# Optimization experiments

Measured on AMD Instinct MI355X. Metric: run time of the kernel, lower is better.

Reference implementation:

```python
import jax, jax.numpy as jnp
import numpy as np

N_NODES = 50000
N_EDGES = 600000
NUM_RELS = 5
IN_CH = 768
HID = 128
OUT_CH = 128
REL_DIM = 200


def _segment_softmax(scores, seg, n):
    # numerically stable softmax over variable-size segments (destination nodes)
    m = jax.ops.segment_max(scores, seg, num_segments=n)
    e = jnp.exp(scores - m[seg])
    s = jax.ops.segment_sum(e, seg, num_segments=n)
    return e / s[seg]


def _hgn_conv(x, edge_index, edge_type, W, Wr, a, Wres, rel_tab, final):
    # x: [N, h_in]; W: [h, h_in]; Wr: [h, rel_dim]; a: [3h]; rel_tab: [R, rel_dim]
    src = edge_index[0]
    dst = edge_index[1]
    n = x.shape[0]
    h = W.shape[0]
    Wx = x @ W.T                      # [N, h] (shared by x_i, x_j, messages)
    rel = rel_tab[edge_type] @ Wr.T   # [E, h]
    aA, aB, aC = a[:h], a[h:2 * h], a[2 * h:]
    # a([Wx_i | Wx_j | Wr rel]) decomposed to avoid materializing the concat
    score = Wx[dst] @ aA + Wx[src] @ aB + rel @ aC   # [E]
    alpha = jax.nn.leaky_relu(score, 0.2)
    alpha = _segment_softmax(alpha, dst, n)
    agg = jax.ops.segment_sum(Wx[src] * alpha[:, None], dst, num_segments=n)
    out = jax.nn.elu(agg + x @ Wres.T)
    if final:
        out = out / jnp.maximum(jnp.linalg.norm(out, axis=1, keepdims=True), 1e-12)
    return out, alpha


def setup_inputs() -> dict:
    key = jax.random.key(0)
    ks = jax.random.split(key, 20)
    s = 0.02
    return {
        "x": jax.random.normal(ks[0], (N_NODES, IN_CH), jnp.float32),
        "edge_index": jax.random.randint(ks[1], (2, N_EDGES), 0, N_NODES, jnp.int64 if jax.config.jax_enable_x64 else jnp.int32),
        "edge_type": jax.random.randint(ks[2], (N_EDGES,), 0, NUM_RELS, jnp.int64 if jax.config.jax_enable_x64 else jnp.int32),
        "l1_W": jax.random.normal(ks[3], (HID, IN_CH), jnp.float32) * s,
        "l1_b": jnp.zeros((HID,), jnp.float32),
        "l2_W": jax.random.normal(ks[4], (OUT_CH, HID), jnp.float32) * s,
        "l2_b": jnp.zeros((OUT_CH,), jnp.float32),
        "W1": jax.random.normal(ks[5], (HID, HID), jnp.float32) * s,
        "Wr1": jax.random.normal(ks[6], (HID, REL_DIM), jnp.float32) * s,
        "a1": jax.random.normal(ks[7], (3 * HID,), jnp.float32) * s,
        "Wres1": jax.random.normal(ks[8], (HID, HID), jnp.float32) * s,
        "rel1": jax.random.normal(ks[9], (NUM_RELS, REL_DIM), jnp.float32),
        "W2": jax.random.normal(ks[10], (HID, HID), jnp.float32) * s,
        "Wr2": jax.random.normal(ks[11], (HID, REL_DIM), jnp.float32) * s,
        "a2": jax.random.normal(ks[12], (3 * HID,), jnp.float32) * s,
        "Wres2": jax.random.normal(ks[13], (HID, HID), jnp.float32) * s,
        "rel2": jax.random.normal(ks[14], (NUM_RELS, REL_DIM), jnp.float32),
    }


def reference(x, edge_index, edge_type, l1_W, l1_b, l2_W, l2_b,
              W1, Wr1, a1, Wres1, rel1, W2, Wr2, a2, Wres2, rel2):
    out = jax.nn.leaky_relu(x @ l1_W.T + l1_b, 0.01)
    # layer 1 (dropout is identity in eval mode)
    out, alpha = _hgn_conv(out, edge_index, edge_type, W1, Wr1, a1, Wres1, rel1, final=False)
    # layer 2: original code blends alpha into self.alpha but weights messages
    # with its own (unblended) softmax alpha, so pre_alpha does not affect output
    out, _ = _hgn_conv(out, edge_index, edge_type, W2, Wr2, a2, Wres2, rel2, final=True)
    out = jax.nn.leaky_relu(out @ l2_W.T + l2_b, 0.01)
    return out
```

## Files before the change

### kernel.cpp

```cpp
#include <hip/hip_runtime.h>

namespace {

typedef unsigned short ushort_t;
typedef unsigned int uint_t;
typedef __attribute__((ext_vector_type(8))) short bf16x8;
typedef __attribute__((ext_vector_type(4))) float f32x4;

constexpr int N   = 50000;
constexpr int E   = 600000;
constexpr int NR  = 5;
constexpr int KIN = 768;
constexpr int H   = 128;
constexpr int RD  = 200;

__device__ inline ushort_t f2b(float f){
  uint_t u = __builtin_bit_cast(uint_t, f);
  uint_t r = (u + 0x7FFFu + ((u >> 16) & 1u)) >> 16;
  return (ushort_t)r;
}
__device__ inline float b2f_lo(uint_t u){ return __builtin_bit_cast(float, u << 16); }
__device__ inline float b2f_hi(uint_t u){ return __builtin_bit_cast(float, u & 0xFFFF0000u); }
__device__ inline float b2f_us(ushort_t h){ return __builtin_bit_cast(float, ((uint_t)h) << 16); }
__device__ inline uint_t cvtpk(float lo, float hi){
  uint_t r;
  asm("v_cvt_pk_bf16_f32 %0, %1, %2" : "=v"(r) : "v"(lo), "v"(hi));
  return r;
}

__global__ void prep_k(const float* __restrict__ l1W, const float* __restrict__ W1,
                       const float* __restrict__ R1, const float* __restrict__ W2,
                       const float* __restrict__ R2, const float* __restrict__ l2W,
                       ushort_t* __restrict__ wts, int* __restrict__ deg,
                       const float* __restrict__ rel1, const float* __restrict__ Wr1,
                       const float* __restrict__ a1, float* __restrict__ sC1,
                       const float* __restrict__ rel2, const float* __restrict__ Wr2,
                       const float* __restrict__ a2, float* __restrict__ sC2){
  constexpr int S0 = H * KIN;
  constexpr int S1 = H * H;
  int b = blockIdx.x, tid = threadIdx.x;
  if (b < 704){
    int i = b * 256 + tid;
    float v;
    if (i < S0) v = l1W[i];
    else {
      int j = i - S0, seg = j >> 14, off = j & (S1 - 1);
      const float* srcs[5] = {W1, R1, W2, R2, l2W};
      v = srcs[seg][off];
    }
    wts[i] = f2b(v);
  } else if (b < 900){
    int i = (b - 704) * 256 + tid;
    if (i < N) deg[i] = 0;
  } else {
    int L = b - 900;
    const float* rel = L ? rel2 : rel1;
    const float* Wr  = L ? Wr2  : Wr1;
    const float* a   = L ? a2   : a1;
    float*       sC  = L ? sC2  : sC1;
    __shared__ float red[256];
    int n = tid >> 1, half = tid & 1;
    float aC = a[256 + n];
    for (int r = 0; r < NR; ++r){
      float p = 0.f;
      for (int k = half * 100; k < half * 100 + 100; ++k)
        p += rel[r * RD + k] * Wr[n * RD + k];
      red[tid] = p * aC;
      __syncthreads();
      for (int s = 128; s > 0; s >>= 1){
        if (tid < s) red[tid] += red[tid + s];
        __syncthreads();
      }
      if (tid == 0) sC[r] = red[0];
      __syncthreads();
    }
  }
}

__global__ void degcount_k(const int* __restrict__ dst, int* __restrict__ deg){
  int e = blockIdx.x * 256 + threadIdx.x;
  if (e < E) atomicAdd(&deg[dst[e]], 1);
}

__global__ void scan1_k(const int* __restrict__ deg, int* __restrict__ chunk,
                        int* __restrict__ bsums, int n){
  __shared__ int s[256];
  int tid = threadIdx.x, i = blockIdx.x * 256 + tid;
  int v = (i < n) ? deg[i] : 0;
  s[tid] = v; __syncthreads();
  for (int off = 1; off < 256; off <<= 1){
    int t = (tid >= off) ? s[tid - off] : 0;
    __syncthreads();
    s[tid] += t;
    __syncthreads();
  }
  if (i < n) chunk[i] = s[tid] - v;
  if (tid == 255) bsums[blockIdx.x] = s[255];
}

__global__ void scan2_k(const int* __restrict__ bsums, int* __restrict__ boffs, int nb){
  __shared__ int s[256];
  int tid = threadIdx.x;
  int v = (tid < nb) ? bsums[tid] : 0;
  s[tid] = v; __syncthreads();
  for (int off = 1; off < 256; off <<= 1){
    int t = (tid >= off) ? s[tid - off] : 0;
    __syncthreads();
    s[tid] += t;
    __syncthreads();
  }
  if (tid < nb) boffs[tid] = s[tid] - v;
}

__global__ void scan3_k(int* __restrict__ rowptr, const int* __restrict__ boffs,
                        int* __restrict__ cursor, int n, int total){
  int i = blockIdx.x * 256 + threadIdx.x;
  if (i < n){
    int v = rowptr[i] + boffs[blockIdx.x];
    rowptr[i] = v; cursor[i] = v;
  }
  if (i == 0) rowptr[n] = total;
}

__global__ void fill_k(const int* __restrict__ src, const int* __restrict__ dst,
                       const int* __restrict__ et, int* __restrict__ cursor,
                       int* __restrict__ cpk){
  int e = blockIdx.x * 256 + threadIdx.x;
  if (e < E){
    int d = dst[e];
    int p = atomicAdd(&cursor[d], 1);
    cpk[p] = src[e] | (et[e] << 16);
  }
}

template<int K1, int M1, bool AFP32, bool NORM, bool STORE1, int M2>
__global__ __launch_bounds__(256) void gfused_k(
    const void* __restrict__ Ap, const ushort_t* __restrict__ Wb1,
    const float* __restrict__ bias1, const ushort_t* __restrict__ aggM,
    ushort_t* __restrict__ out1,
    const ushort_t* __restrict__ Wb2, const float* __restrict__ vec2,
    void* __restrict__ out2, float* __restrict__ sA, float* __restrict__ sB, int M)
{
  constexpr int AP = 40;
  constexpr int BP = 40;
  constexpr int CP = 136;
  __shared__ __align__(16) ushort_t U[128 * CP];
  __shared__ __align__(16) ushort_t Cs[64 * CP];
  ushort_t* const As  = U;
  ushort_t* const Bs  = U + 64 * AP;
  ushort_t* const B2s = U;
  const int tid  = threadIdx.x;
  const int wave = tid >> 6, lane = tid & 63;
  const int l15  = lane & 15, quad = lane >> 4;
  const int row0 = blockIdx.x * 64;

  if (M1 == 2){
    #pragma unroll
    for (int i = 0; i < 4; ++i){
      int idx = tid + 256 * i;
      int r = idx >> 4, c8 = idx & 15;
      int grow = row0 + r;
      uint4 v = make_uint4(0, 0, 0, 0);
      if (grow < M) v = *reinterpret_cast<const uint4*>(aggM + (size_t)grow * 128 + c8 * 8);
      *reinterpret_cast<uint4*>(&Cs[r * CP + c8 * 8]) = v;
    }
  }

  f32x4 acc[8];
  #pragma unroll
  for (int t = 0; t < 8; ++t) acc[t] = (f32x4){0.f, 0.f, 0.f, 0.f};

  const int ar = tid >> 2, aq = tid & 3;
  const int agrow = row0 + ar;
  const bool aok = agrow < M;
  const int bn = tid >> 1, bs16 = (tid & 1) * 16;

  float4 pf0 = make_float4(0.f, 0.f, 0.f, 0.f), pf1 = pf0;
  uint4  pu  = make_uint4(0, 0, 0, 0);
  uint4  pb0, pb1;

  if (AFP32){
    if (aok){
      const float* ap = (const float*)Ap + (size_t)agrow * K1 + aq * 8;
      pf0 = *reinterpret_cast<const float4*>(ap);
      pf1 = *reinterpret_cast<const float4*>(ap + 4);
    }
  } else if (aok){
    pu = *reinterpret_cast<const uint4*>((const ushort_t*)Ap + (size_t)agrow * K1 + aq * 8);
  }
  {
    const ushort_t* wp = Wb1 + (size_t)bn * K1 + bs16;
    pb0 = *reinterpret_cast<const uint4*>(wp);
    pb1 = *reinterpret_cast<const uint4*>(wp + 8);
  }

  for (int k0 = 0; k0 < K1; k0 += 32){
    uint4 av;
    if (AFP32){
      av.x = cvtpk(pf0.x, pf0.y); av.y = cvtpk(pf0.z, pf0.w);
      av.z = cvtpk(pf1.x, pf1.y); av.w = cvtpk(pf1.z, pf1.w);
    } else av = pu;
    *reinterpret_cast<uint4*>(&As[ar * AP + aq * 8]) = av;
    *reinterpret_cast<uint4*>(&Bs[bn * BP + bs16])     = pb0;
    *reinterpret_cast<uint4*>(&Bs[bn * BP + bs16 + 8]) = pb1;
    __syncthreads();
    if (k0 + 32 < K1){
      const int k1 = k0 + 32;
      if (AFP32){
        if (aok){
          const float* ap = (const float*)Ap + (size_t)agrow * K1 + k1 + aq * 8;
          pf0 = *reinterpret_cast<const float4*>(ap);
          pf1 = *reinterpret_cast<const float4*>(ap + 4);
        }
      } else if (aok){
        pu = *reinterpret_cast<const uint4*>((const ushort_t*)Ap + (size_t)agrow * K1 + k1 + aq * 8);
      }
      const ushort_t* wp = Wb1 + (size_t)bn * K1 + k1 + bs16;
      pb0 = *reinterpret_cast<const uint4*>(wp);
      pb1 = *reinterpret_cast<const uint4*>(wp + 8);
    }
    bf16x8 af = *reinterpret_cast<const bf16x8*>(&As[(wave * 16 + l15) * AP + quad * 8]);
    #pragma unroll
    for (int t = 0; t < 8; ++t){
      bf16x8 bfr = *reinterpret_cast<const bf16x8*>(&Bs[(t * 16 + l15) * BP + quad * 8]);
      acc[t] = __builtin_amdgcn_mfma_f32_16x16x32_bf16(af, bfr, acc[t], 0, 0, 0);
    }
    __syncthreads();
  }

  uint4 wreg[8];
  #pragma unroll
  for (int i = 0; i < 8; ++i){
    int idx = tid + 256 * i;
    int rr = idx >> 4, c8 = idx & 15;
    wreg[i] = *reinterpret_cast<const uint4*>(Wb2 + (size_t)rr * 128 + c8 * 8);
  }

  float vv[8][4];
  #pragma unroll
  for (int t = 0; t < 8; ++t){
    #pragma unroll
    for (int r = 0; r < 4; ++r){
      int lr  = wave * 16 + quad * 4 + r;
      int col = t * 16 + l15;
      float v = acc[t][r];
      if (M1 == 1){
        v += bias1[col];
        v = v > 0.f ? v : 0.01f * v;
      } else {
        v += b2f_us(Cs[lr * CP + col]);
        v = v > 0.f ? v : __expf(v) - 1.f;
      }
      vv[t][r] = v;
    }
  }
  #pragma unroll
  for (int i = 0; i < 8; ++i){
    int idx = tid + 256 * i;
    int rr = idx >> 4, c8 = idx & 15;
    *reinterpret_cast<uint4*>(&B2s[rr * CP + c8 * 8]) = wreg[i];
  }
  if (NORM){
    #pragma unroll
    for (int r = 0; r < 4; ++r){
      float ss = 0.f;
      #pragma unroll
      for (int t = 0; t < 8; ++t) ss += vv[t][r] * vv[t][r];
      #pragma unroll
      for (int off = 1; off < 16; off <<= 1) ss += __shfl_xor(ss, off, 64);
      float sc = 1.f / fmaxf(sqrtf(ss), 1e-12f);
      #pragma unroll
      for (int t = 0; t < 8; ++t) vv[t][r] *= sc;
    }
  }
  #pragma unroll
  for (int t = 0; t < 8; t += 2){
    #pragma unroll
    for (int r = 0; r < 4; ++r){
      int lr  = wave * 16 + quad * 4 + r;
      int c0  = t * 16 + l15, c1 = c0 + 16;
      uint_t pr = cvtpk(vv[t][r], vv[t + 1][r]);
      Cs[lr * CP + c0] = (ushort_t)pr;
      Cs[lr * CP + c1] = (ushort_t)(pr >> 16);
      if (STORE1){
        int grow = row0 + lr;
        if (grow < M){
          out1[(size_t)grow * 128 + c0] = (ushort_t)pr;
          out1[(size_t)grow * 128 + c1] = (ushort_t)(pr >> 16);
        }
      }
    }
  }
  __syncthreads();

  #pragma unroll
  for (int t = 0; t < 8; ++t) acc[t] = (f32x4){0.f, 0.f, 0.f, 0.f};
  #pragma unroll
  for (int kk = 0; kk < 4; ++kk){
    bf16x8 af2 = *reinterpret_cast<const bf16x8*>(&Cs[(wave * 16 + l15) * CP + kk * 32 + quad * 8]);
    #pragma unroll
    for (int t = 0; t < 8; ++t){
      bf16x8 bfr = *reinterpret_cast<const bf16x8*>(&B2s[(t * 16 + l15) * CP + kk * 32 + quad * 8]);
      acc[t] = __builtin_amdgcn_mfma_f32_16x16x32_bf16(af2, bfr, acc[t], 0, 0, 0);
    }
  }

  if (M2 == 1){
    #pragma unroll
    for (int t = 0; t < 8; ++t){
      #pragma unroll
      for (int r = 0; r < 4; ++r){
        int grow = row0 + wave * 16 + quad * 4 + r;
        if (grow >= M) continue;
        int col = t * 16 + l15;
        float v = acc[t][r] + vec2[col];
        v = v > 0.f ? v : 0.01f * v;
        ((float*)out2)[(size_t)grow * 128 + col] = v;
      }
    }
  } else {
    #pragma unroll
    for (int t = 0; t < 8; t += 2){
      #pragma unroll
      for (int r = 0; r < 4; ++r){
        int grow = row0 + wave * 16 + quad * 4 + r;
        if (grow >= M) continue;
        int c0 = t * 16 + l15;
        uint_t pr = cvtpk(acc[t][r], acc[t + 1][r]);
        ((ushort_t*)out2)[(size_t)grow * 128 + c0]      = (ushort_t)pr;
        ((ushort_t*)out2)[(size_t)grow * 128 + c0 + 16] = (ushort_t)(pr >> 16);
      }
    }
    #pragma unroll
    for (int r = 0; r < 4; ++r){
      float pa = 0.f, pb = 0.f;
      #pragma unroll
      for (int t = 0; t < 8; ++t){
        int col = t * 16 + l15;
        pa += acc[t][r] * vec2[col];
        pb += acc[t][r] * vec2[128 + col];
      }
      #pragma unroll
      for (int off = 1; off < 16; off <<= 1){
        pa += __shfl_xor(pa, off, 64);
        pb += __shfl_xor(pb, off, 64);
      }
      int grow = row0 + wave * 16 + quad * 4 + r;
      if (l15 == r && grow < M){ sA[grow] = pa; sB[grow] = pb; }
    }
  }
}

__global__ __launch_bounds__(256) void agg_k(
    const ushort_t* __restrict__ Wx, const float* __restrict__ sA,
    const float* __restrict__ sB, const float* __restrict__ sC,
    const int* __restrict__ rowptr, const int* __restrict__ cpk,
    uint_t* __restrict__ aggU, int n)
{
  const int node  = blockIdx.x * 16 + (threadIdx.x >> 4);
  const int l     = threadIdx.x & 15;
  const int gbase = threadIdx.x & 48;
  if (node >= n) return;
  int p0 = rowptr[node], p1 = rowptr[node + 1];
  int deg = p1 - p0;
  float sa = sA[node];
  float m = -1e30f, ssum = 0.f;
  float a[8];
  #pragma unroll
  for (int j = 0; j < 8; ++j) a[j] = 0.f;

  for (int c0 = 0; c0 < deg; c0 += 16){
    int cnt = deg - c0; if (cnt > 16) cnt = 16;
    bool ok = l < cnt;
    int pk = cpk[p0 + c0 + (ok ? l : 0)];
    float s = sa + sB[pk & 0xFFFF] + sC[pk >> 16];
    s = s > 0.f ? s : 0.2f * s;
    float sv = ok ? s : -1e30f;
    #pragma unroll
    for (int off = 8; off > 0; off >>= 1) sv = fmaxf(sv, __shfl_xor(sv, off, 16));
    float mn = fmaxf(m, sv);
    float corr = __expf(m - mn);
    ssum *= corr;
    #pragma unroll
    for (int j = 0; j < 8; ++j) a[j] *= corr;
    float ev = ok ? __expf(s - mn) : 0.f;
    float es = ev;
    #pragma unroll
    for (int off = 8; off > 0; off >>= 1) es += __shfl_xor(es, off, 16);
    ssum += es;
    m = mn;
    int png = ok ? pk : 0;

    for (int e = 0; e < cnt; e += 4){
      int b0l = gbase + e;
      int pe0 = __shfl(png, b0l,     64), pe1 = __shfl(png, b0l + 1, 64);
      int pe2 = __shfl(png, b0l + 2, 64), pe3 = __shfl(png, b0l + 3, 64);
      float e0 = __shfl(ev, b0l,     64), e1 = __shfl(ev, b0l + 1, 64);
      float e2 = __shfl(ev, b0l + 2, 64), e3 = __shfl(ev, b0l + 3, 64);
      uint4 u0 = *reinterpret_cast<const uint4*>(Wx + (size_t)(pe0 & 0xFFFF) * 128 + l * 8);
      uint4 u1 = *reinterpret_cast<const uint4*>(Wx + (size_t)(pe1 & 0xFFFF) * 128 + l * 8);
      uint4 u2 = *reinterpret_cast<const uint4*>(Wx + (size_t)(pe2 & 0xFFFF) * 128 + l * 8);
      uint4 u3 = *reinterpret_cast<const uint4*>(Wx + (size_t)(pe3 & 0xFFFF) * 128 + l * 8);
      a[0] += e0 * b2f_lo(u0.x); a[1] += e0 * b2f_hi(u0.x);
      a[2] += e0 * b2f_lo(u0.y); a[3] += e0 * b2f_hi(u0.y);
      a[4] += e0 * b2f_lo(u0.z); a[5] += e0 * b2f_hi(u0.z);
      a[6] += e0 * b2f_lo(u0.w); a[7] += e0 * b2f_hi(u0.w);
      a[0] += e1 * b2f_lo(u1.x); a[1] += e1 * b2f_hi(u1.x);
      a[2] += e1 * b2f_lo(u1.y); a[3] += e1 * b2f_hi(u1.y);
      a[4] += e1 * b2f_lo(u1.z); a[5] += e1 * b2f_hi(u1.z);
      a[6] += e1 * b2f_lo(u1.w); a[7] += e1 * b2f_hi(u1.w);
      a[0] += e2 * b2f_lo(u2.x); a[1] += e2 * b2f_hi(u2.x);
      a[2] += e2 * b2f_lo(u2.y); a[3] += e2 * b2f_hi(u2.y);
      a[4] += e2 * b2f_lo(u2.z); a[5] += e2 * b2f_hi(u2.z);
      a[6] += e2 * b2f_lo(u2.w); a[7] += e2 * b2f_hi(u2.w);
      a[0] += e3 * b2f_lo(u3.x); a[1] += e3 * b2f_hi(u3.x);
      a[2] += e3 * b2f_lo(u3.y); a[3] += e3 * b2f_hi(u3.y);
      a[4] += e3 * b2f_lo(u3.z); a[5] += e3 * b2f_hi(u3.z);
      a[6] += e3 * b2f_lo(u3.w); a[7] += e3 * b2f_hi(u3.w);
    }
  }
  float inv = (deg > 0) ? 1.f / ssum : 0.f;
  uint4 o;
  o.x = cvtpk(a[0] * inv, a[1] * inv);
  o.y = cvtpk(a[2] * inv, a[3] * inv);
  o.z = cvtpk(a[4] * inv, a[5] * inv);
  o.w = cvtpk(a[6] * inv, a[7] * inv);
  *reinterpret_cast<uint4*>(aggU + (size_t)node * 64 + l * 4) = o;
}

}

extern "C" void kernel_launch(void* const* d_in, const int* in_sizes, int n_in,
                              void* d_out, int out_size, void* d_ws, size_t ws_size,
                              hipStream_t stream)
{
  const float* x     = (const float*)d_in[0];
  const int*   eidx  = (const int*)d_in[1];
  const int*   et    = (const int*)d_in[2];
  const float* l1W   = (const float*)d_in[3];
  const float* l1b   = (const float*)d_in[4];
  const float* l2W   = (const float*)d_in[5];
  const float* l2b   = (const float*)d_in[6];
  const float* W1    = (const float*)d_in[7];
  const float* Wr1   = (const float*)d_in[8];
  const float* a1    = (const float*)d_in[9];
  const float* Wres1 = (const float*)d_in[10];
  const float* rel1  = (const float*)d_in[11];
  const float* W2    = (const float*)d_in[12];
  const float* Wr2   = (const float*)d_in[13];
  const float* a2    = (const float*)d_in[14];
  const float* Wres2 = (const float*)d_in[15];
  const float* rel2  = (const float*)d_in[16];
  float* outp = (float*)d_out;

  const int* esrc = eidx;
  const int* edst = eidx + E;

  float* f = (float*)d_ws;
  size_t o = 0;
  float* sA   = f + o; o += N;
  float* sB   = f + o; o += N;
  float* sC1  = f + o; o += 8;
  float* sC2  = f + o; o += 8;
  ushort_t* us = (ushort_t*)(f + o);
  size_t ou = 0;
  ushort_t* b0   = us + ou; ou += (size_t)N * H;
  ushort_t* b1   = us + ou; ou += (size_t)N * H;
  ushort_t* Wxb  = us + ou; ou += (size_t)N * H;
  ushort_t* aggB = us + ou; ou += (size_t)N * H;
  ushort_t* wtsb = us + ou; ou += (size_t)H * KIN + 5 * H * H;
  ushort_t* l1Wb = wtsb;
  ushort_t* W1b  = wtsb + H * KIN;
  ushort_t* R1b  = W1b + H * H;
  ushort_t* W2b  = R1b + H * H;
  ushort_t* R2b  = W2b + H * H;
  ushort_t* l2Wb = R2b + H * H;
  if (ou & 1) ou += 1;
  int* wi = (int*)(us + ou);
  size_t oi = 0;
  int* deg    = wi + oi; oi += N;
  int* rowptr = wi + oi; oi += N + 1;
  int* cursor = wi + oi; oi += N;
  int* bsums  = wi + oi; oi += 256;
  int* boffs  = wi + oi; oi += 256;
  int* cpk    = wi + oi; oi += E;

  const int EB    = (E + 255) / 256;
  const int NB256 = (N + 255) / 256;
  const int GB    = (N + 63) / 64;
  const int NB16  = (N + 15) / 16;

  prep_k<<<902, 256, 0, stream>>>(l1W, W1, Wres1, W2, Wres2, l2W, wtsb, deg,
                                  rel1, Wr1, a1, sC1, rel2, Wr2, a2, sC2);
  degcount_k<<<EB, 256, 0, stream>>>(edst, deg);
  scan1_k<<<NB256, 256, 0, stream>>>(deg, rowptr, bsums, N);
  scan2_k<<<1, 256, 0, stream>>>(bsums, boffs, NB256);
  scan3_k<<<NB256, 256, 0, stream>>>(rowptr, boffs, cursor, N, E);
  fill_k<<<EB, 256, 0, stream>>>(esrc, edst, et, cursor, cpk);

  gfused_k<KIN, 1, true, false, true, 3><<<GB, 256, 0, stream>>>(
      x, l1Wb, l1b, nullptr, b0, W1b, a1, Wxb, sA, sB, N);
  agg_k<<<NB16, 256, 0, stream>>>(Wxb, sA, sB, sC1, rowptr, cpk, (uint_t*)aggB, N);

  gfused_k<H, 2, false, false, true, 3><<<GB, 256, 0, stream>>>(
      b0, R1b, nullptr, aggB, b1, W2b, a2, Wxb, sA, sB, N);
  agg_k<<<NB16, 256, 0, stream>>>(Wxb, sA, sB, sC2, rowptr, cpk, (uint_t*)aggB, N);

  gfused_k<H, 2, false, true, false, 1><<<GB, 256, 0, stream>>>(
      b1, R2b, nullptr, aggB, nullptr, l2Wb, l2b, outp, nullptr, nullptr, N);
}
```

Before: 495.0 us.

## Load GEMM operands directly from global into MFMA registers, drop LDS staging

```diff
diff --git a/kernel.cpp b/kernel.cpp
--- a/kernel.cpp
+++ b/kernel.cpp
@@ -134,131 +134,74 @@
 }
 
 template<int K1, int M1, bool AFP32, bool NORM, bool STORE1, int M2>
-__global__ __launch_bounds__(256) void gfused_k(
+__global__ __launch_bounds__(256, 3) void gfused_k(
     const void* __restrict__ Ap, const ushort_t* __restrict__ Wb1,
     const float* __restrict__ bias1, const ushort_t* __restrict__ aggM,
     ushort_t* __restrict__ out1,
     const ushort_t* __restrict__ Wb2, const float* __restrict__ vec2,
     void* __restrict__ out2, float* __restrict__ sA, float* __restrict__ sB, int M)
 {
-  constexpr int AP = 40;
-  constexpr int BP = 40;
-  constexpr int CP = 136;
-  __shared__ __align__(16) ushort_t U[128 * CP];
-  __shared__ __align__(16) ushort_t Cs[64 * CP];
-  ushort_t* const As  = U;
-  ushort_t* const Bs  = U + 64 * AP;
-  ushort_t* const B2s = U;
+  __shared__ __align__(16) ushort_t Cs[64 * 128];
   const int tid  = threadIdx.x;
   const int wave = tid >> 6, lane = tid & 63;
   const int l15  = lane & 15, quad = lane >> 4;
   const int row0 = blockIdx.x * 64;
-
-  if (M1 == 2){
-    #pragma unroll
-    for (int i = 0; i < 4; ++i){
-      int idx = tid + 256 * i;
-      int r = idx >> 4, c8 = idx & 15;
-      int grow = row0 + r;
-      uint4 v = make_uint4(0, 0, 0, 0);
-      if (grow < M) v = *reinterpret_cast<const uint4*>(aggM + (size_t)grow * 128 + c8 * 8);
-      *reinterpret_cast<uint4*>(&Cs[r * CP + c8 * 8]) = v;
-    }
-  }
+  const int arow_l = wave * 16 + l15;
+  int ar = row0 + arow_l; if (ar >= M) ar = M - 1;
 
   f32x4 acc[8];
   #pragma unroll
   for (int t = 0; t < 8; ++t) acc[t] = (f32x4){0.f, 0.f, 0.f, 0.f};
 
-  const int ar = tid >> 2, aq = tid & 3;
-  const int agrow = row0 + ar;
-  const bool aok = agrow < M;
-  const int bn = tid >> 1, bs16 = (tid & 1) * 16;
-
-  float4 pf0 = make_float4(0.f, 0.f, 0.f, 0.f), pf1 = pf0;
-  uint4  pu  = make_uint4(0, 0, 0, 0);
-  uint4  pb0, pb1;
-
+  const ushort_t* wb = Wb1 + (size_t)l15 * K1 + quad * 8;
   if (AFP32){
-    if (aok){
-      const float* ap = (const float*)Ap + (size_t)agrow * K1 + aq * 8;
-      pf0 = *reinterpret_cast<const float4*>(ap);
-      pf1 = *reinterpret_cast<const float4*>(ap + 4);
-    }
-  } else if (aok){
-    pu = *reinterpret_cast<const uint4*>((const ushort_t*)Ap + (size_t)agrow * K1 + aq * 8);
-  }
-  {
-    const ushort_t* wp = Wb1 + (size_t)bn * K1 + bs16;
-    pb0 = *reinterpret_cast<const uint4*>(wp);
-    pb1 = *reinterpret_cast<const uint4*>(wp + 8);
-  }
-
-  for (int k0 = 0; k0 < K1; k0 += 32){
-    uint4 av;
-    if (AFP32){
-      av.x = cvtpk(pf0.x, pf0.y); av.y = cvtpk(pf0.z, pf0.w);
-      av.z = cvtpk(pf1.x, pf1.y); av.w = cvtpk(pf1.z, pf1.w);
-    } else av = pu;
-    *reinterpret_cast<uint4*>(&As[ar * AP + aq * 8]) = av;
-    *reinterpret_cast<uint4*>(&Bs[bn * BP + bs16])     = pb0;
-    *reinterpret_cast<uint4*>(&Bs[bn * BP + bs16 + 8]) = pb1;
-    __syncthreads();
-    if (k0 + 32 < K1){
-      const int k1 = k0 + 32;
-      if (AFP32){
-        if (aok){
-          const float* ap = (const float*)Ap + (size_t)agrow * K1 + k1 + aq * 8;
-          pf0 = *reinterpret_cast<const float4*>(ap);
-          pf1 = *reinterpret_cast<const float4*>(ap + 4);
-        }
-      } else if (aok){
-        pu = *reinterpret_cast<const uint4*>((const ushort_t*)Ap + (size_t)agrow * K1 + k1 + aq * 8);
-      }
-      const ushort_t* wp = Wb1 + (size_t)bn * K1 + k1 + bs16;
-      pb0 = *reinterpret_cast<const uint4*>(wp);
-      pb1 = *reinterpret_cast<const uint4*>(wp + 8);
-    }
-    bf16x8 af = *reinterpret_cast<const bf16x8*>(&As[(wave * 16 + l15) * AP + quad * 8]);
-    #pragma unroll
-    for (int t = 0; t < 8; ++t){
-      bf16x8 bfr = *reinterpret_cast<const bf16x8*>(&Bs[(t * 16 + l15) * BP + quad * 8]);
-      acc[t] = __builtin_amdgcn_mfma_f32_16x16x32_bf16(af, bfr, acc[t], 0, 0, 0);
-    }
-    __syncthreads();
-  }
-
-  uint4 wreg[8];
-  #pragma unroll
-  for (int i = 0; i < 8; ++i){
-    int idx = tid + 256 * i;
-    int rr = idx >> 4, c8 = idx & 15;
-    wreg[i] = *reinterpret_cast<const uint4*>(Wb2 + (size_t)rr * 128 + c8 * 8);
-  }
-
+    const float* ap = (const float*)Ap + (size_t)ar * K1 + quad * 8;
+    #pragma unroll 2
+    for (int k0 = 0; k0 < K1; k0 += 32){
+      float4 u0 = *reinterpret_cast<const float4*>(ap + k0);
+      float4 u1 = *reinterpret_cast<const float4*>(ap + k0 + 4);
+      uint4 av;
+      av.x = cvtpk(u0.x, u0.y); av.y = cvtpk(u0.z, u0.w);
+      av.z = cvtpk(u1.x, u1.y); av.w = cvtpk(u1.z, u1.w);
+      bf16x8 af = __builtin_bit_cast(bf16x8, av);
+      #pragma unroll
+      for (int t = 0; t < 8; ++t){
+        bf16x8 bfr = *reinterpret_cast<const bf16x8*>(wb + (size_t)t * 16 * K1 + k0);
+        acc[t] = __builtin_amdgcn_mfma_f32_16x16x32_bf16(af, bfr, acc[t], 0, 0, 0);
+      }
+    }
+  } else {
+    const ushort_t* apb = (const ushort_t*)Ap + (size_t)ar * K1 + quad * 8;
+    #pragma unroll 2
+    for (int k0 = 0; k0 < K1; k0 += 32){
+      bf16x8 af = *reinterpret_cast<const bf16x8*>(apb + k0);
+      #pragma unroll
+      for (int t = 0; t < 8; ++t){
+        bf16x8 bfr = *reinterpret_cast<const bf16x8*>(wb + (size_t)t * 16 * K1 + k0);
+        acc[t] = __builtin_amdgcn_mfma_f32_16x16x32_bf16(af, bfr, acc[t], 0, 0, 0);
+      }
+    }
+  }
+
+  const int lr0 = wave * 16 + quad * 4;
   float vv[8][4];
   #pragma unroll
   for (int t = 0; t < 8; ++t){
     #pragma unroll
     for (int r = 0; r < 4; ++r){
-      int lr  = wave * 16 + quad * 4 + r;
       int col = t * 16 + l15;
       float v = acc[t][r];
       if (M1 == 1){
         v += bias1[col];
         v = v > 0.f ? v : 0.01f * v;
       } else {
-        v += b2f_us(Cs[lr * CP + col]);
+        int g = row0 + lr0 + r;
+        float ag = (g < M) ? b2f_us(aggM[(size_t)g * 128 + col]) : 0.f;
+        v += ag;
         v = v > 0.f ? v : __expf(v) - 1.f;
       }
       vv[t][r] = v;
     }
-  }
-  #pragma unroll
-  for (int i = 0; i < 8; ++i){
-    int idx = tid + 256 * i;
-    int rr = idx >> 4, c8 = idx & 15;
-    *reinterpret_cast<uint4*>(&B2s[rr * CP + c8 * 8]) = wreg[i];
   }
   if (NORM){
     #pragma unroll
@@ -277,16 +220,18 @@
   for (int t = 0; t < 8; t += 2){
     #pragma unroll
     for (int r = 0; r < 4; ++r){
-      int lr  = wave * 16 + quad * 4 + r;
-      int c0  = t * 16 + l15, c1 = c0 + 16;
+      int row = lr0 + r;
+      int key = row & 7;
       uint_t pr = cvtpk(vv[t][r], vv[t + 1][r]);
-      Cs[lr * CP + c0] = (ushort_t)pr;
-      Cs[lr * CP + c1] = (ushort_t)(pr >> 16);
+      int c0 = t * 16 + l15, c1 = c0 + 16;
+      int p0 = ((c0 >> 3) ^ key) << 3, p1 = ((c1 >> 3) ^ key) << 3;
+      Cs[row * 128 + p0 + (l15 & 7)] = (ushort_t)pr;
+      Cs[row * 128 + p1 + (l15 & 7)] = (ushort_t)(pr >> 16);
       if (STORE1){
-        int grow = row0 + lr;
-        if (grow < M){
-          out1[(size_t)grow * 128 + c0] = (ushort_t)pr;
-          out1[(size_t)grow * 128 + c1] = (ushort_t)(pr >> 16);
+        int g = row0 + row;
+        if (g < M){
+          out1[(size_t)g * 128 + c0] = (ushort_t)pr;
+          out1[(size_t)g * 128 + c1] = (ushort_t)(pr >> 16);
         }
       }
     }
@@ -295,22 +240,28 @@
 
   #pragma unroll
   for (int t = 0; t < 8; ++t) acc[t] = (f32x4){0.f, 0.f, 0.f, 0.f};
-  #pragma unroll
-  for (int kk = 0; kk < 4; ++kk){
-    bf16x8 af2 = *reinterpret_cast<const bf16x8*>(&Cs[(wave * 16 + l15) * CP + kk * 32 + quad * 8]);
+  {
+    const int rr   = wave * 16 + l15;
+    const int rkey = l15 & 7;
+    const ushort_t* w2 = Wb2 + (size_t)l15 * 128 + quad * 8;
+    #pragma unroll 2
+    for (int kk = 0; kk < 4; ++kk){
+      int ph = (((kk * 4 + quad) ^ rkey) << 3);
+      bf16x8 af2 = *reinterpret_cast<const bf16x8*>(&Cs[rr * 128 + ph]);
+      #pragma unroll
+      for (int t = 0; t < 8; ++t){
+        bf16x8 bfr = *reinterpret_cast<const bf16x8*>(w2 + (size_t)t * 16 * 128 + kk * 32);
+        acc[t] = __builtin_amdgcn_mfma_f32_16x16x32_bf16(af2, bfr, acc[t], 0, 0, 0);
+      }
+    }
+  }
+
+  if (M2 == 1){
     #pragma unroll
     for (int t = 0; t < 8; ++t){
-      bf16x8 bfr = *reinterpret_cast<const bf16x8*>(&B2s[(t * 16 + l15) * CP + kk * 32 + quad * 8]);
-      acc[t] = __builtin_amdgcn_mfma_f32_16x16x32_bf16(af2, bfr, acc[t], 0, 0, 0);
-    }
-  }
-
-  if (M2 == 1){
-    #pragma unroll
-    for (int t = 0; t < 8; ++t){
       #pragma unroll
       for (int r = 0; r < 4; ++r){
-        int grow = row0 + wave * 16 + quad * 4 + r;
+        int grow = row0 + lr0 + r;
         if (grow >= M) continue;
         int col = t * 16 + l15;
         float v = acc[t][r] + vec2[col];
@@ -323,7 +274,7 @@
     for (int t = 0; t < 8; t += 2){
       #pragma unroll
       for (int r = 0; r < 4; ++r){
-        int grow = row0 + wave * 16 + quad * 4 + r;
+        int grow = row0 + lr0 + r;
         if (grow >= M) continue;
         int c0 = t * 16 + l15;
         uint_t pr = cvtpk(acc[t][r], acc[t + 1][r]);
@@ -345,7 +296,7 @@
         pa += __shfl_xor(pa, off, 64);
         pb += __shfl_xor(pb, off, 64);
       }
-      int grow = row0 + wave * 16 + quad * 4 + r;
+      int grow = row0 + lr0 + r;
       if (l15 == r && grow < M){ sA[grow] = pa; sB[grow] = pb; }
     }
   }
```

Measured after the change: 575.2 us. +16.2%, slower.

## Fuse edge softmax aggregation into the following GEMM kernel and merge degree count into prep

Applied to the files above, without the earlier changes.

```diff
diff --git a/kernel.cpp b/kernel.cpp
--- a/kernel.cpp
+++ b/kernel.cpp
@@ -32,6 +32,7 @@
                        const float* __restrict__ R1, const float* __restrict__ W2,
                        const float* __restrict__ R2, const float* __restrict__ l2W,
                        ushort_t* __restrict__ wts, int* __restrict__ deg,
+                       const int* __restrict__ edst,
                        const float* __restrict__ rel1, const float* __restrict__ Wr1,
                        const float* __restrict__ a1, float* __restrict__ sC1,
                        const float* __restrict__ rel2, const float* __restrict__ Wr2,
@@ -49,11 +50,8 @@
       v = srcs[seg][off];
     }
     wts[i] = f2b(v);
-  } else if (b < 900){
-    int i = (b - 704) * 256 + tid;
-    if (i < N) deg[i] = 0;
-  } else {
-    int L = b - 900;
+  } else if (b < 706){
+    int L = b - 704;
     const float* rel = L ? rel2 : rel1;
     const float* Wr  = L ? Wr2  : Wr1;
     const float* a   = L ? a2   : a1;
@@ -74,12 +72,10 @@
       if (tid == 0) sC[r] = red[0];
       __syncthreads();
     }
-  }
-}
-
-__global__ void degcount_k(const int* __restrict__ dst, int* __restrict__ deg){
-  int e = blockIdx.x * 256 + threadIdx.x;
-  if (e < E) atomicAdd(&deg[dst[e]], 1);
+  } else {
+    int e = (b - 706) * 256 + tid;
+    if (e < E) atomicAdd(&deg[edst[e]], 1);
+  }
 }
 
 __global__ void scan1_k(const int* __restrict__ deg, int* __restrict__ chunk,
@@ -136,10 +132,13 @@
 template<int K1, int M1, bool AFP32, bool NORM, bool STORE1, int M2>
 __global__ __launch_bounds__(256) void gfused_k(
     const void* __restrict__ Ap, const ushort_t* __restrict__ Wb1,
-    const float* __restrict__ bias1, const ushort_t* __restrict__ aggM,
+    const float* __restrict__ bias1,
+    const ushort_t* __restrict__ WxG, const int* __restrict__ rowptr,
+    const int* __restrict__ cpk, const float* __restrict__ sAi,
+    const float* __restrict__ sBi, const float* __restrict__ sCi,
     ushort_t* __restrict__ out1,
     const ushort_t* __restrict__ Wb2, const float* __restrict__ vec2,
-    void* __restrict__ out2, float* __restrict__ sA, float* __restrict__ sB, int M)
+    void* __restrict__ out2, float* __restrict__ sAo, float* __restrict__ sBo, int M)
 {
   constexpr int AP = 40;
   constexpr int BP = 40;
@@ -155,14 +154,78 @@
   const int row0 = blockIdx.x * 64;
 
   if (M1 == 2){
-    #pragma unroll
-    for (int i = 0; i < 4; ++i){
-      int idx = tid + 256 * i;
-      int r = idx >> 4, c8 = idx & 15;
-      int grow = row0 + r;
-      uint4 v = make_uint4(0, 0, 0, 0);
-      if (grow < M) v = *reinterpret_cast<const uint4*>(aggM + (size_t)grow * 128 + c8 * 8);
-      *reinterpret_cast<uint4*>(&Cs[r * CP + c8 * 8]) = v;
+    const int grp = tid >> 4;
+    const int l   = tid & 15;
+    const int gb  = tid & 48;
+    #pragma unroll 1
+    for (int nb = 0; nb < 4; ++nb){
+      int lrow = nb * 16 + grp;
+      int node = row0 + lrow;
+      uint4 o = make_uint4(0, 0, 0, 0);
+      if (node < M){
+        int p0 = rowptr[node], p1 = rowptr[node + 1];
+        int dg = p1 - p0;
+        float sa = sAi[node];
+        float m = -1e30f, ssum = 0.f;
+        float a[8];
+        #pragma unroll
+        for (int j = 0; j < 8; ++j) a[j] = 0.f;
+        for (int c0 = 0; c0 < dg; c0 += 16){
+          int cnt = dg - c0; if (cnt > 16) cnt = 16;
+          bool ok = l < cnt;
+          int pk = cpk[p0 + c0 + (ok ? l : 0)];
+          float s = sa + sBi[pk & 0xFFFF] + sCi[pk >> 16];
+          s = s > 0.f ? s : 0.2f * s;
+          float sv = ok ? s : -1e30f;
+          #pragma unroll
+          for (int off = 8; off > 0; off >>= 1) sv = fmaxf(sv, __shfl_xor(sv, off, 16));
+          float mn = fmaxf(m, sv);
+          float corr = __expf(m - mn);
+          ssum *= corr;
+          #pragma unroll
+          for (int j = 0; j < 8; ++j) a[j] *= corr;
+          float ev = ok ? __expf(s - mn) : 0.f;
+          float es = ev;
+          #pragma unroll
+          for (int off = 8; off > 0; off >>= 1) es += __shfl_xor(es, off, 16);
+          ssum += es;
+          m = mn;
+          int png = ok ? pk : 0;
+          for (int e = 0; e < cnt; e += 4){
+            int b0l = gb + e;
+            int pe0 = __shfl(png, b0l,     64), pe1 = __shfl(png, b0l + 1, 64);
+            int pe2 = __shfl(png, b0l + 2, 64), pe3 = __shfl(png, b0l + 3, 64);
+            float e0 = __shfl(ev, b0l,     64), e1 = __shfl(ev, b0l + 1, 64);
+            float e2 = __shfl(ev, b0l + 2, 64), e3 = __shfl(ev, b0l + 3, 64);
+            uint4 u0 = *reinterpret_cast<const uint4*>(WxG + (size_t)(pe0 & 0xFFFF) * 128 + l * 8);
+            uint4 u1 = *reinterpret_cast<const uint4*>(WxG + (size_t)(pe1 & 0xFFFF) * 128 + l * 8);
+            uint4 u2 = *reinterpret_cast<const uint4*>(WxG + (size_t)(pe2 & 0xFFFF) * 128 + l * 8);
+            uint4 u3 = *reinterpret_cast<const uint4*>(WxG + (size_t)(pe3 & 0xFFFF) * 128 + l * 8);
+            a[0] += e0 * b2f_lo(u0.x); a[1] += e0 * b2f_hi(u0.x);
+            a[2] += e0 * b2f_lo(u0.y); a[3] += e0 * b2f_hi(u0.y);
+            a[4] += e0 * b2f_lo(u0.z); a[5] += e0 * b2f_hi(u0.z);
+            a[6] += e0 * b2f_lo(u0.w); a[7] += e0 * b2f_hi(u0.w);
+            a[0] += e1 * b2f_lo(u1.x); a[1] += e1 * b2f_hi(u1.x);
+            a[2] += e1 * b2f_lo(u1.y); a[3] += e1 * b2f_hi(u1.y);
+            a[4] += e1 * b2f_lo(u1.z); a[5] += e1 * b2f_hi(u1.z);
+            a[6] += e1 * b2f_lo(u1.w); a[7] += e1 * b2f_hi(u1.w);
+            a[0] += e2 * b2f_lo(u2.x); a[1] += e2 * b2f_hi(u2.x);
+            a[2] += e2 * b2f_lo(u2.y); a[3] += e2 * b2f_hi(u2.y);
+            a[4] += e2 * b2f_lo(u2.z); a[5] += e2 * b2f_hi(u2.z);
+            a[6] += e2 * b2f_lo(u2.w); a[7] += e2 * b2f_hi(u2.w);
+            a[0] += e3 * b2f_lo(u3.x); a[1] += e3 * b2f_hi(u3.x);
+            a[2] += e3 * b2f_lo(u3.y); a[3] += e3 * b2f_hi(u3.y);
+            a[4] += e3 * b2f_lo(u3.z); a[5] += e3 * b2f_hi(u3.z);
+            a[6] += e3 * b2f_lo(u3.w); a[7] += e3 * b2f_hi(u3.w);
+          }
+        }
+        float inv = (dg > 0) ? 1.f / ssum : 0.f;
+        o.x = cvtpk(a[0] * inv, a[1] * inv);
+        o.y = cvtpk(a[2] * inv, a[3] * inv);
+        o.z = cvtpk(a[4] * inv, a[5] * inv);
+        o.w = cvtpk(a[6] * inv, a[7] * inv);
+      }
+      *reinterpret_cast<uint4*>(&Cs[lrow * CP + l * 8]) = o;
     }
   }
 
@@ -346,86 +409,9 @@
         pb += __shfl_xor(pb, off, 64);
       }
       int grow = row0 + wave * 16 + quad * 4 + r;
-      if (l15 == r && grow < M){ sA[grow] = pa; sB[grow] = pb; }
-    }
-  }
-}
-
-__global__ __launch_bounds__(256) void agg_k(
-    const ushort_t* __restrict__ Wx, const float* __restrict__ sA,
-    const float* __restrict__ sB, const float* __restrict__ sC,
-    const int* __restrict__ rowptr, const int* __restrict__ cpk,
-    uint_t* __restrict__ aggU, int n)
-{
-  const int node  = blockIdx.x * 16 + (threadIdx.x >> 4);
-  const int l     = threadIdx.x & 15;
-  const int gbase = threadIdx.x & 48;
-  if (node >= n) return;
-  int p0 = rowptr[node], p1 = rowptr[node + 1];
-  int deg = p1 - p0;
-  float sa = sA[node];
-  float m = -1e30f, ssum = 0.f;
-  float a[8];
-  #pragma unroll
-  for (int j = 0; j < 8; ++j) a[j] = 0.f;
-
-  for (int c0 = 0; c0 < deg; c0 += 16){
-    int cnt = deg - c0; if (cnt > 16) cnt = 16;
-    bool ok = l < cnt;
-    int pk = cpk[p0 + c0 + (ok ? l : 0)];
-    float s = sa + sB[pk & 0xFFFF] + sC[pk >> 16];
-    s = s > 0.f ? s : 0.2f * s;
-    float sv = ok ? s : -1e30f;
-    #pragma unroll
-    for (int off = 8; off > 0; off >>= 1) sv = fmaxf(sv, __shfl_xor(sv, off, 16));
-    float mn = fmaxf(m, sv);
-    float corr = __expf(m - mn);
-    ssum *= corr;
-    #pragma unroll
-    for (int j = 0; j < 8; ++j) a[j] *= corr;
-    float ev = ok ? __expf(s - mn) : 0.f;
-    float es = ev;
-    #pragma unroll
-    for (int off = 8; off > 0; off >>= 1) es += __shfl_xor(es, off, 16);
-    ssum += es;
-    m = mn;
-    int png = ok ? pk : 0;
-
-    for (int e = 0; e < cnt; e += 4){
-      int b0l = gbase + e;
-      int pe0 = __shfl(png, b0l,     64), pe1 = __shfl(png, b0l + 1, 64);
-      int pe2 = __shfl(png, b0l + 2, 64), pe3 = __shfl(png, b0l + 3, 64);
-      float e0 = __shfl(ev, b0l,     64), e1 = __shfl(ev, b0l + 1, 64);
-      float e2 = __shfl(ev, b0l + 2, 64), e3 = __shfl(ev, b0l + 3, 64);
-      uint4 u0 = *reinterpret_cast<const uint4*>(Wx + (size_t)(pe0 & 0xFFFF) * 128 + l * 8);
-      uint4 u1 = *reinterpret_cast<const uint4*>(Wx + (size_t)(pe1 & 0xFFFF) * 128 + l * 8);
-      uint4 u2 = *reinterpret_cast<const uint4*>(Wx + (size_t)(pe2 & 0xFFFF) * 128 + l * 8);
-      uint4 u3 = *reinterpret_cast<const uint4*>(Wx + (size_t)(pe3 & 0xFFFF) * 128 + l * 8);
-      a[0] += e0 * b2f_lo(u0.x); a[1] += e0 * b2f_hi(u0.x);
-      a[2] += e0 * b2f_lo(u0.y); a[3] += e0 * b2f_hi(u0.y);
-      a[4] += e0 * b2f_lo(u0.z); a[5] += e0 * b2f_hi(u0.z);
-      a[6] += e0 * b2f_lo(u0.w); a[7] += e0 * b2f_hi(u0.w);
-      a[0] += e1 * b2f_lo(u1.x); a[1] += e1 * b2f_hi(u1.x);
-      a[2] += e1 * b2f_lo(u1.y); a[3] += e1 * b2f_hi(u1.y);
-      a[4] += e1 * b2f_lo(u1.z); a[5] += e1 * b2f_hi(u1.z);
-      a[6] += e1 * b2f_lo(u1.w); a[7] += e1 * b2f_hi(u1.w);
-      a[0] += e2 * b2f_lo(u2.x); a[1] += e2 * b2f_hi(u2.x);
-      a[2] += e2 * b2f_lo(u2.y); a[3] += e2 * b2f_hi(u2.y);
-      a[4] += e2 * b2f_lo(u2.z); a[5] += e2 * b2f_hi(u2.z);
-      a[6] += e2 * b2f_lo(u2.w); a[7] += e2 * b2f_hi(u2.w);
-      a[0] += e3 * b2f_lo(u3.x); a[1] += e3 * b2f_hi(u3.x);
-      a[2] += e3 * b2f_lo(u3.y); a[3] += e3 * b2f_hi(u3.y);
-      a[4] += e3 * b2f_lo(u3.z); a[5] += e3 * b2f_hi(u3.z);
-      a[6] += e3 * b2f_lo(u3.w); a[7] += e3 * b2f_hi(u3.w);
-    }
-  }
-  float inv = (deg > 0) ? 1.f / ssum : 0.f;
-  uint4 o;
-  o.x = cvtpk(a[0] * inv, a[1] * inv);
-  o.y = cvtpk(a[2] * inv, a[3] * inv);
-  o.z = cvtpk(a[4] * inv, a[5] * inv);
-  o.w = cvtpk(a[6] * inv, a[7] * inv);
-  *reinterpret_cast<uint4*>(aggU + (size_t)node * 64 + l * 4) = o;
+      if (l15 == r && grow < M){ sAo[grow] = pa; sBo[grow] = pb; }
+    }
+  }
 }
 
 }
@@ -458,16 +444,18 @@
 
   float* f = (float*)d_ws;
   size_t o = 0;
-  float* sA   = f + o; o += N;
-  float* sB   = f + o; o += N;
+  float* sA1  = f + o; o += N;
+  float* sB1  = f + o; o += N;
+  float* sA2  = f + o; o += N;
+  float* sB2  = f + o; o += N;
   float* sC1  = f + o; o += 8;
   float* sC2  = f + o; o += 8;
   ushort_t* us = (ushort_t*)(f + o);
   size_t ou = 0;
   ushort_t* b0   = us + ou; ou += (size_t)N * H;
   ushort_t* b1   = us + ou; ou += (size_t)N * H;
-  ushort_t* Wxb  = us + ou; ou += (size_t)N * H;
-  ushort_t* aggB = us + ou; ou += (size_t)N * H;
+  ushort_t* WxA  = us + ou; ou += (size_t)N * H;
+  ushort_t* WxB  = us + ou; ou += (size_t)N * H;
   ushort_t* wtsb = us + ou; ou += (size_t)H * KIN + 5 * H * H;
   ushort_t* l1Wb = wtsb;
   ushort_t* W1b  = wtsb + H * KIN;
@@ -488,24 +476,24 @@
   const int EB    = (E + 255) / 256;
   const int NB256 = (N + 255) / 256;
   const int GB    = (N + 63) / 64;
-  const int NB16  = (N + 15) / 16;
-
-  prep_k<<<902, 256, 0, stream>>>(l1W, W1, Wres1, W2, Wres2, l2W, wtsb, deg,
-                                  rel1, Wr1, a1, sC1, rel2, Wr2, a2, sC2);
-  degcount_k<<<EB, 256, 0, stream>>>(edst, deg);
+
+  hipMemsetAsync(deg, 0, (size_t)N * sizeof(int), stream);
+  prep_k<<<706 + EB, 256, 0, stream>>>(l1W, W1, Wres1, W2, Wres2, l2W, wtsb, deg,
+                                       edst, rel1, Wr1, a1, sC1, rel2, Wr2, a2, sC2);
   scan1_k<<<NB256, 256, 0, stream>>>(deg, rowptr, bsums, N);
   scan2_k<<<1, 256, 0, stream>>>(bsums, boffs, NB256);
   scan3_k<<<NB256, 256, 0, stream>>>(rowptr, boffs, cursor, N, E);
   fill_k<<<EB, 256, 0, stream>>>(esrc, edst, et, cursor, cpk);
 
   gfused_k<KIN, 1, true, false, true, 3><<<GB, 256, 0, stream>>>(
-      x, l1Wb, l1b, nullptr, b0, W1b, a1, Wxb, sA, sB, N);
-  agg_k<<<NB16, 256, 0, stream>>>(Wxb, sA, sB, sC1, rowptr, cpk, (uint_t*)aggB, N);
+      x, l1Wb, l1b, nullptr, nullptr, nullptr, nullptr, nullptr, nullptr,
+      b0, W1b, a1, WxA, sA1, sB1, N);
 
   gfused_k<H, 2, false, false, true, 3><<<GB, 256, 0, stream>>>(
-      b0, R1b, nullptr, aggB, b1, W2b, a2, Wxb, sA, sB, N);
-  agg_k<<<NB16, 256, 0, stream>>>(Wxb, sA, sB, sC2, rowptr, cpk, (uint_t*)aggB, N);
+      b0, R1b, nullptr, WxA, rowptr, cpk, sA1, sB1, sC1,
+      b1, W2b, a2, WxB, sA2, sB2, N);
 
   gfused_k<H, 2, false, true, false, 1><<<GB, 256, 0, stream>>>(
-      b1, R2b, nullptr, aggB, nullptr, l2Wb, l2b, outp, nullptr, nullptr, N);
-}
+      b1, R2b, nullptr, WxB, rowptr, cpk, sA2, sB2, sC2,
+      nullptr, l2Wb, l2b, outp, nullptr, nullptr, N);
+}
```

New measurement: 501.5 us. About the same (+1.3%).
